# Kernel optimization log

Hardware: AMD Instinct MI355X
Metric: run time of the kernel (lower is better)

Reference implementation:

```python
import jax, jax.numpy as jnp
import numpy as np

B = 32768
D = 1024          # input_dim
SEL = 512         # select_dim (per-expert selected features)
E = 6             # num_experts
K = 3             # top_k
SH = 32           # shared_dim
INNER = 64        # cross-attn inner dim (4 heads * 16)
HID = 128         # expert hidden


def setup_inputs() -> dict:
    key = jax.random.key(0)
    ks = jax.random.split(key, 16)
    s = lambda i, shape, scale=0.02: (jax.random.normal(ks[i], shape, jnp.float32) * scale)
    return {
        "x": jax.random.normal(ks[0], (B, D), jnp.float32),
        # CrossAttention(query_dim=512, context_dim=512, heads=4, dim_head=16)
        "Wq": s(1, (512, INNER)),
        "Wk": s(2, (512, INNER)),
        "Wv": s(3, (512, INNER)),
        "Wo": s(4, (INNER, 512)),
        "bo": jnp.zeros((512,), jnp.float32),
        # shared_proj: Linear(512, 32)
        "Wsp": s(5, (512, SH)),
        "bsp": jnp.zeros((SH,), jnp.float32),
        # gate: Linear(1024, 6)
        "Wg": s(6, (D, E)),
        "bg": jnp.zeros((E,), jnp.float32),
        # per-expert feature-mask logits
        "mask_logits": jax.random.normal(ks[7], (E, D), jnp.float32),
        # expert MLPs: Linear(544,128) -> ReLU -> Linear(128,1), stacked over experts
        "W1": s(8, (E, SEL + SH, HID)),
        "b1": jnp.zeros((E, HID), jnp.float32),
        "W2": s(9, (E, HID, 1)),
        "b2": jnp.zeros((E, 1), jnp.float32),
    }


def _moe_forward(x, Wq, Wk, Wv, Wo, bo, Wsp, bsp, Wg, bg, mask_logits, W1, b1, W2, b2):
    x_sem = x[:, :512]
    x_vis = x[:, 512:]

    # CrossAttention with a single query token attending to a single context
    # token: softmax over one key is identically 1, so attn output == v.
    v = x_vis @ Wv                      # [B, INNER]
    shared_token = v @ Wo + bo          # to_out Linear, [B, 512]
    shared_info = shared_token @ Wsp + bsp  # [B, SH]

    # Gating: top-k experts per sample, softmax over selected logits
    gate_logits = x @ Wg + bg                       # [B, E]
    topk_scores, topk_idx = jax.lax.top_k(gate_logits, K)  # [B, K]
    topk_w = jax.nn.softmax(topk_scores, axis=1)    # [B, K]

    # Per-expert learned feature selection (top-512 of sigmoid(mask_logits));
    # sigmoid is monotonic but kept for faithfulness.
    mask_prob = jax.nn.sigmoid(mask_logits)         # [E, D]
    _, sel_idx = jax.lax.top_k(mask_prob, SEL)      # [E, SEL]

    # Dense expert evaluation (every expert on every sample), then gather the
    # routed outputs -- same math as the original scatter loop.
    x_sel = jnp.take(x, sel_idx, axis=1)            # [B, E, SEL]
    h = jnp.einsum('bes,esh->beh', x_sel, W1[:, :SEL, :])
    h = h + jnp.einsum('bd,edh->beh', shared_info, W1[:, SEL:, :])
    h = jax.nn.relu(h + b1[None])                   # [B, E, HID]
    expert_out = jnp.einsum('beh,eh->be', h, W2[:, :, 0]) + b2[None, :, 0]  # [B, E]

    routed = jnp.take_along_axis(expert_out, topk_idx, axis=1)  # [B, K]
    return jnp.sum(topk_w * routed, axis=1, keepdims=True)      # [B, 1]


def reference(x, Wq, Wk, Wv, Wo, bo, Wsp, bsp, Wg, bg, mask_logits, W1, b1, W2, b2):
    return _moe_forward(x, Wq, Wk, Wv, Wo, bo, Wsp, bsp, Wg, bg, mask_logits, W1, b1, W2, b2)
```

## Files before the change

### kernel.cpp

```cpp
#include <hip/hip_runtime.h>

#define B 32768
#define D 1024
#define SEL 512
#define E 6
#define K 3
#define SH 32
#define HID 128
#define NKT 16

typedef __attribute__((ext_vector_type(8))) short bf16x8;
typedef __attribute__((ext_vector_type(4))) float f32x4;

__device__ __forceinline__ unsigned short f2bf(float f) {
  unsigned u = __float_as_uint(f);
  return (unsigned short)((u + 0x7fffu + ((u >> 16) & 1u)) >> 16);
}
__device__ __forceinline__ float bf2f(unsigned short h) {
  return __uint_as_float((unsigned)h << 16);
}

__device__ __forceinline__ void gload_lds16(const void* g, void* l) {
  __builtin_amdgcn_global_load_lds(
      (const __attribute__((address_space(1))) void*)g,
      (__attribute__((address_space(3))) void*)l, 16, 0, 0);
}

__global__ void k_sel(const float* __restrict__ ml, int* __restrict__ inv,
                      int* __restrict__ cnt) {
  __shared__ float row[D];
  const int e = blockIdx.x, t = threadIdx.x;
  if (t == 0) cnt[e] = 0;
  row[t] = ml[e * D + t];
  __syncthreads();
  const float v = row[t];
  int rank = 0;
  for (int i = 0; i < D; ++i) {
    float u = row[i];
    rank += (u > v) || (u == v && i < t);
  }
  inv[e * D + t] = (rank < SEL) ? rank : -1;
}

__global__ __launch_bounds__(256) void k_wowsp(
    const float* __restrict__ Wo, const float* __restrict__ Wsp,
    const float* __restrict__ bo, const float* __restrict__ bsp,
    const float* __restrict__ Wg,
    float* __restrict__ WoWsp, float* __restrict__ bfull,
    unsigned short* __restrict__ WgS) {
  __shared__ float red[256];
  const int t = threadIdx.x;
  const int j = t & 31, chunk = t >> 5;
  const int blk = blockIdx.x;
  if (blk < 64) {
    const int i = blk;
    float p = 0.f;
    for (int c = chunk * 64; c < chunk * 64 + 64; ++c)
      p += Wo[i * 512 + c] * Wsp[c * SH + j];
    red[t] = p;
    __syncthreads();
    if (t < 32) {
      float s = 0.f;
      #pragma unroll
      for (int k = 0; k < 8; ++k) s += red[k * 32 + j];
      WoWsp[i * SH + j] = s;
    }
  } else if (blk == 64) {
    float p = 0.f;
    for (int c = chunk * 64; c < chunk * 64 + 64; ++c)
      p += bo[c] * Wsp[c * SH + j];
    red[t] = p;
    __syncthreads();
    if (t < 32) {
      float s = bsp[j];
      #pragma unroll
      for (int k = 0; k < 8; ++k) s += red[k * 32 + j];
      bfull[j] = s;
    }
  } else {
    const int idx = (blk - 65) * 256 + t;
    const int col = idx >> 10, k = idx & 1023;
    float wv = (col < E) ? Wg[(size_t)k * E + col] : 0.f;
    unsigned short hi = f2bf(wv);
    unsigned short lo = f2bf(wv - bf2f(hi));
    WgS[col * D + k] = hi;
    WgS[16 * D + col * D + k] = lo;
  }
}

__global__ __launch_bounds__(256) void k_wfull2(
    const float* __restrict__ Wv, const float* __restrict__ WoWsp,
    float* __restrict__ Wfull) {
  __shared__ float wsh[64 * SH];
  const int t = threadIdx.x;
  for (int idx = t; idx < 64 * SH; idx += 256) wsh[idx] = WoWsp[idx];
  __syncthreads();
  const int c = blockIdx.x * 8 + (t >> 5), j = t & 31;
  float p = 0.f;
  #pragma unroll 8
  for (int i = 0; i < 64; ++i) p += Wv[c * 64 + i] * wsh[i * SH + j];
  Wfull[c * SH + j] = p;
}

__global__ __launch_bounds__(256) void k_w1c(
    const float* __restrict__ W1, const float* __restrict__ b1,
    const int* __restrict__ inv, const float* __restrict__ Wfull,
    const float* __restrict__ bfull,
    unsigned short* __restrict__ W1eT, float* __restrict__ b1c) {
  __shared__ float w1b[SH];
  __shared__ float bf[SH];
  const int e = blockIdx.x >> 7, h = blockIdx.x & 127;
  const int t = threadIdx.x;
  const float* We = W1 + (size_t)e * (SEL + SH) * HID;
  if (t < SH) { w1b[t] = We[(size_t)(SEL + t) * HID + h]; bf[t] = bfull[t]; }
  __syncthreads();
  const int* iv = inv + e * D;
  unsigned short* dst = W1eT + ((size_t)e * HID + h) * D;
  #pragma unroll
  for (int it = 0; it < 4; ++it) {
    int d = t + it * 256;
    int s = iv[d];
    float v = (s >= 0) ? We[(size_t)s * HID + h] : 0.f;
    if (d >= 512) {
      const float* wf = Wfull + (size_t)(d - 512) * SH;
      float p = 0.f;
      #pragma unroll
      for (int j = 0; j < SH; ++j) p += wf[j] * w1b[j];
      v += p;
    }
    dst[d] = f2bf(v);
  }
  if (t == 0) {
    float p = b1[e * HID + h];
    for (int j = 0; j < SH; ++j) p += bf[j] * w1b[j];
    b1c[e * HID + h] = p;
  }
}

template<bool WRITE_XBF>
__global__ __launch_bounds__(256) void k_xgate(
    const float* __restrict__ x, const unsigned short* __restrict__ WgS,
    const float* __restrict__ Wg, const float* __restrict__ bg,
    unsigned short* __restrict__ xbf,
    int* __restrict__ cnt, int* __restrict__ clist, float* __restrict__ wlist) {
  __shared__ __align__(16) char ldsAh[64 * 128];
  __shared__ __align__(16) char ldsAl[64 * 128];
  __shared__ __align__(16) char ldsW[4096];
  __shared__ float gl_s[64][8];
  const int t = threadIdx.x;
  const int bm = blockIdx.x;
  const int w = t >> 6, lane = t & 63;
  const int g = lane >> 4, j = lane & 15;
  const int swz = ((lane & 7) * 16) ^ ((lane >> 3) << 4);

  const char* srcW = (const char*)WgS +
                     (size_t)(w * 8 + (lane >> 3)) * (D * 2) + swz;

  f32x4 acc = {0.f, 0.f, 0.f, 0.f};

  for (int kt = 0; kt < NKT; ++kt) {
    if (kt) __syncthreads();
    gload_lds16(srcW + kt * 128, ldsW + w * 1024);
    #pragma unroll
    for (int it = 0; it < 4; ++it) {
      int r = (t >> 4) + it * 16;
      const float4 v =
          *(const float4*)(x + (size_t)(bm * 64 + r) * D + kt * 64 + (t & 15) * 4);
      ushort4 hh, ll;
      hh.x = f2bf(v.x); hh.y = f2bf(v.y); hh.z = f2bf(v.z); hh.w = f2bf(v.w);
      ll.x = f2bf(v.x - bf2f(hh.x)); ll.y = f2bf(v.y - bf2f(hh.y));
      ll.z = f2bf(v.z - bf2f(hh.z)); ll.w = f2bf(v.w - bf2f(hh.w));
      if (WRITE_XBF)
        *(ushort4*)(xbf + (size_t)(bm * 64 + r) * D + kt * 64 + (t & 15) * 4) = hh;
      const int ao = r * 128 + (((t & 15) * 8) ^ ((r & 7) << 4));
      *(ushort4*)(ldsAh + ao) = hh;
      *(ushort4*)(ldsAl + ao) = ll;
    }
    __syncthreads();
    #pragma unroll
    for (int kk = 0; kk < 2; ++kk) {
      const int kb = kk * 64 + g * 16;
      const int wo = kb ^ ((j & 7) << 4);
      bf16x8 bh = *(const bf16x8*)(ldsW + j * 128 + wo);
      bf16x8 bl = *(const bf16x8*)(ldsW + 2048 + j * 128 + wo);
      const int row = w * 16 + j;
      const int aoff = row * 128 + (kb ^ ((row & 7) << 4));
      bf16x8 ah = *(const bf16x8*)(ldsAh + aoff);
      bf16x8 al = *(const bf16x8*)(ldsAl + aoff);
      acc = __builtin_amdgcn_mfma_f32_16x16x32_bf16(ah, bh, acc, 0, 0, 0);
      acc = __builtin_amdgcn_mfma_f32_16x16x32_bf16(ah, bl, acc, 0, 0, 0);
      acc = __builtin_amdgcn_mfma_f32_16x16x32_bf16(al, bh, acc, 0, 0, 0);
      acc = __builtin_amdgcn_mfma_f32_16x16x32_bf16(al, bl, acc, 0, 0, 0);
    }
  }
  if (j < E) {
    #pragma unroll
    for (int ri = 0; ri < 4; ++ri)
      gl_s[w * 16 + g * 4 + ri][j] = acc[ri];
  }
  __syncthreads();
  if (t < 64) {
    const int tok = bm * 64 + t;
    float gv[E];
    #pragma unroll
    for (int e2 = 0; e2 < E; ++e2) gv[e2] = gl_s[t][e2] + bg[e2];

    float s4[4];
    {
      bool used[E] = {};
      #pragma unroll
      for (int k = 0; k < 4; ++k) {
        float best = -1e30f; int bi = 0;
        for (int e2 = 0; e2 < E; ++e2)
          if (!used[e2] && gv[e2] > best) { best = gv[e2]; bi = e2; }
        used[bi] = true; s4[k] = best;
      }
    }
    unsigned long long flags = __ballot(s4[2] - s4[3] < 4e-3f);
    while (flags) {
      const int fl = __ffsll((long long)flags) - 1;
      flags &= flags - 1;
      const int tokf = bm * 64 + fl;
      float ex[E] = {};
      for (int i = 0; i < 16; ++i) {
        const int d = t + 64 * i;
        float xv = x[(size_t)tokf * D + d];
        const float* wr = Wg + (size_t)d * E;
        #pragma unroll
        for (int e2 = 0; e2 < E; ++e2) ex[e2] += xv * wr[e2];
      }
      #pragma unroll
      for (int e2 = 0; e2 < E; ++e2) {
        float s = ex[e2];
        s += __shfl_xor(s, 1); s += __shfl_xor(s, 2); s += __shfl_xor(s, 4);
        s += __shfl_xor(s, 8); s += __shfl_xor(s, 16); s += __shfl_xor(s, 32);
        ex[e2] = s;
      }
      if (t == fl) {
        #pragma unroll
        for (int e2 = 0; e2 < E; ++e2) gv[e2] = ex[e2] + bg[e2];
      }
    }
    int idx[K]; float sc[K];
    bool used[E] = {};
    #pragma unroll
    for (int k = 0; k < K; ++k) {
      float best = -1e30f; int bi = 0;
      for (int e2 = 0; e2 < E; ++e2)
        if (!used[e2] && gv[e2] > best) { best = gv[e2]; bi = e2; }
      used[bi] = true; sc[k] = best; idx[k] = bi;
    }
    float s1 = __expf(sc[1] - sc[0]), s2 = __expf(sc[2] - sc[0]);
    float inv_s = 1.f / (1.f + s1 + s2);
    float tw[K] = {inv_s, s1 * inv_s, s2 * inv_s};
    const unsigned long long below = (1ULL << t) - 1ULL;
    #pragma unroll
    for (int e2 = 0; e2 < E; ++e2) {
      int myk = -1;
      #pragma unroll
      for (int k = 0; k < K; ++k) if (idx[k] == e2) myk = k;
      unsigned long long m = __ballot(myk >= 0);
      if (m) {
        int tot = __popcll(m);
        int leader = __ffsll((long long)m) - 1;
        int base = 0;
        if (t == leader) base = atomicAdd(&cnt[e2], tot);
        base = __shfl(base, leader);
        if (myk >= 0) {
          int pos = base + __popcll(m & below);
          clist[e2 * B + pos] = (tok << 2) | myk;
          wlist[e2 * B + pos] = tw[myk];
        }
      }
    }
  }
}

template<int AMODE>
__global__ __launch_bounds__(256) void k_gemm(
    const float* __restrict__ x, const unsigned short* __restrict__ xbf,
    const unsigned short* __restrict__ W1eT,
    const int* __restrict__ cnt, const int* __restrict__ clist,
    const float* __restrict__ wlist,
    const float* __restrict__ b1c, const float* __restrict__ W2,
    const float* __restrict__ b2, float* __restrict__ eo4) {
  __shared__ __align__(16) char ldsA[128 * 128];
  __shared__ __align__(16) char ldsB[128 * 128];
  __shared__ int tokl[128];
  __shared__ float red[128];

  const int t = threadIdx.x;
  const int e = blockIdx.x >> 8;
  const int bm = blockIdx.x & 255;
  const int n = cnt[e];
  if (bm * 128 >= n) return;
  const int cb = e * B;

  if (t < 128) {
    int gr = bm * 128 + t;
    tokl[t] = clist[cb + (gr < n ? gr : 0)] >> 2;
  }
  __syncthreads();

  const int w = t >> 6, lane = t & 63;
  const int g = lane >> 4, j = lane & 15;
  const int swz = ((lane & 7) * 16) ^ ((lane >> 3) << 4);

  const char* srcB[4];
  #pragma unroll
  for (int q = 0; q < 4; ++q)
    srcB[q] = (const char*)W1eT +
              (size_t)(e * HID + w * 32 + q * 8 + (lane >> 3)) * (D * 2) + swz;
  const char* srcA[4];
  if (AMODE == 0) {
    #pragma unroll
    for (int q = 0; q < 4; ++q)
      srcA[q] = (const char*)xbf +
                (size_t)tokl[w * 32 + q * 8 + (lane >> 3)] * 2048 + swz;
  }

  f32x4 acc[2][8] = {};

  for (int kt = 0; kt < NKT; ++kt) {
    if (kt) __syncthreads();
    if (AMODE == 0) {
      #pragma unroll
      for (int q = 0; q < 4; ++q)
        gload_lds16(srcA[q] + kt * 128, ldsA + w * 4096 + q * 1024);
    }
    #pragma unroll
    for (int q = 0; q < 4; ++q)
      gload_lds16(srcB[q] + kt * 128, ldsB + w * 4096 + q * 1024);
    if (AMODE == 1) {
      #pragma unroll
      for (int it = 0; it < 8; ++it) {
        int r = (t >> 4) + it * 16;
        const float4 v =
            *(const float4*)(x + (size_t)tokl[r] * D + kt * 64 + (t & 15) * 4);
        ushort4 h4;
        h4.x = f2bf(v.x); h4.y = f2bf(v.y); h4.z = f2bf(v.z); h4.w = f2bf(v.w);
        *(ushort4*)(ldsA + r * 128 + (((t & 15) * 8) ^ ((r & 7) << 4))) = h4;
      }
    }
    __syncthreads();
    #pragma unroll
    for (int kk = 0; kk < 2; ++kk) {
      const int kb = kk * 64 + g * 16;
      bf16x8 aF[2];
      #pragma unroll
      for (int fm = 0; fm < 2; ++fm) {
        int row = w * 32 + fm * 16 + j;
        aF[fm] = *(const bf16x8*)(ldsA + row * 128 + (kb ^ ((row & 7) << 4)));
      }
      #pragma unroll
      for (int fn = 0; fn < 8; ++fn) {
        int col = fn * 16 + j;
        bf16x8 bF = *(const bf16x8*)(ldsB + col * 128 + (kb ^ ((col & 7) << 4)));
        acc[0][fn] = __builtin_amdgcn_mfma_f32_16x16x32_bf16(aF[0], bF, acc[0][fn], 0, 0, 0);
        acc[1][fn] = __builtin_amdgcn_mfma_f32_16x16x32_bf16(aF[1], bF, acc[1][fn], 0, 0, 0);
      }
    }
  }

  float vb1[8], vw2[8];
  #pragma unroll
  for (int fn = 0; fn < 8; ++fn) {
    int col = fn * 16 + j;
    vb1[fn] = b1c[e * HID + col];
    vw2[fn] = W2[e * HID + col];
  }
  #pragma unroll
  for (int fm = 0; fm < 2; ++fm) {
    #pragma unroll
    for (int r = 0; r < 4; ++r) {
      float s = 0.f;
      #pragma unroll
      for (int fn = 0; fn < 8; ++fn)
        s += fmaxf(acc[fm][fn][r] + vb1[fn], 0.f) * vw2[fn];
      s += __shfl_xor(s, 1); s += __shfl_xor(s, 2);
      s += __shfl_xor(s, 4); s += __shfl_xor(s, 8);
      if (j == 0) red[w * 32 + fm * 16 + g * 4 + r] = s;
    }
  }
  __syncthreads();
  if (t < 128) {
    int gr = bm * 128 + t;
    if (gr < n) {
      int en = clist[cb + gr];
      eo4[(size_t)(en >> 2) * 4 + (en & 3)] = wlist[cb + gr] * (red[t] + b2[e]);
    }
  }
}

__global__ void k_comb2(const float* __restrict__ eo4, float* __restrict__ out) {
  const int tok = blockIdx.x * 256 + threadIdx.x;
  float4 v = *(const float4*)(eo4 + (size_t)tok * 4);
  out[tok] = v.x + v.y + v.z;
}

extern "C" void kernel_launch(void* const* d_in, const int* in_sizes, int n_in,
                              void* d_out, int out_size, void* d_ws, size_t ws_size,
                              hipStream_t stream) {
  const float* x   = (const float*)d_in[0];
  const float* Wv  = (const float*)d_in[3];
  const float* Wo  = (const float*)d_in[4];
  const float* bo  = (const float*)d_in[5];
  const float* Wsp = (const float*)d_in[6];
  const float* bsp = (const float*)d_in[7];
  const float* Wg  = (const float*)d_in[8];
  const float* bg  = (const float*)d_in[9];
  const float* ml  = (const float*)d_in[10];
  const float* W1  = (const float*)d_in[11];
  const float* b1  = (const float*)d_in[12];
  const float* W2  = (const float*)d_in[13];
  const float* b2  = (const float*)d_in[14];
  float* out = (float*)d_out;

  char* ws = (char*)d_ws;
  int*   inv   = (int*)ws;
  float* WoWsp = (float*)(ws + 32768);
  float* Wfull = (float*)(ws + 49152);
  float* bfull = (float*)(ws + 114688);
  float* b1c   = (float*)(ws + 118784);
  int*   cnt   = (int*)(ws + 126976);
  unsigned short* WgS = (unsigned short*)(ws + 131072);
  int*   clist = (int*)(ws + 262144);
  float* wlist = (float*)(ws + 1048576);
  float* eo4   = (float*)(ws + 1835008);
  unsigned short* W1eT = (unsigned short*)(ws + 2359296);
  unsigned short* xbf  = (unsigned short*)(ws + 3932160);
  const bool use_xbf = ws_size >= (size_t)3932160 + (size_t)B * D * 2;

  k_sel<<<E, D, 0, stream>>>(ml, inv, cnt);
  k_wowsp<<<129, 256, 0, stream>>>(Wo, Wsp, bo, bsp, Wg, WoWsp, bfull, WgS);
  k_wfull2<<<64, 256, 0, stream>>>(Wv, WoWsp, Wfull);
  k_w1c<<<E * HID, 256, 0, stream>>>(W1, b1, inv, Wfull, bfull, W1eT, b1c);
  if (use_xbf)
    k_xgate<true><<<B / 64, 256, 0, stream>>>(x, WgS, Wg, bg, xbf, cnt, clist, wlist);
  else
    k_xgate<false><<<B / 64, 256, 0, stream>>>(x, WgS, Wg, bg, xbf, cnt, clist, wlist);
  if (use_xbf)
    k_gemm<0><<<E * 256, 256, 0, stream>>>(x, xbf, W1eT, cnt, clist, wlist, b1c, W2, b2, eo4);
  else
    k_gemm<1><<<E * 256, 256, 0, stream>>>(x, xbf, W1eT, cnt, clist, wlist, b1c, W2, b2, eo4);
  k_comb2<<<B / 256, 256, 0, stream>>>(eo4, out);
}
```

Measured before the change: 175.7 us.

## Software-pipeline x and gate-weight loads in the gating kernel

The gating kernel now issues the next k-tile's x float4 loads into registers and its gate-weight tile into a second LDS buffer before running the MFMA work on the current tile. This replaces the old load-then-compute sequence inside each iteration. The goal is to hide global memory latency on the large x read behind the bf16 split and MFMA math. In exchange it uses more registers and an extra 4 KB of LDS, which may reduce occupancy.

```diff
diff --git a/kernel.cpp b/kernel.cpp
--- a/kernel.cpp
+++ b/kernel.cpp
@@ -145,44 +145,66 @@
     int* __restrict__ cnt, int* __restrict__ clist, float* __restrict__ wlist) {
   __shared__ __align__(16) char ldsAh[64 * 128];
   __shared__ __align__(16) char ldsAl[64 * 128];
-  __shared__ __align__(16) char ldsW[4096];
+  __shared__ __align__(16) char ldsW[2][4096];
   __shared__ float gl_s[64][8];
   const int t = threadIdx.x;
   const int bm = blockIdx.x;
   const int w = t >> 6, lane = t & 63;
   const int g = lane >> 4, j = lane & 15;
+  const int tok0 = bm * 64;
   const int swz = ((lane & 7) * 16) ^ ((lane >> 3) << 4);
+  const int r0 = t >> 4, c16 = t & 15;
 
   const char* srcW = (const char*)WgS +
                      (size_t)(w * 8 + (lane >> 3)) * (D * 2) + swz;
 
   f32x4 acc = {0.f, 0.f, 0.f, 0.f};
 
+  gload_lds16(srcW, ldsW[0] + w * 1024);
+  float4 vb0, vb1, vb2, vb3;
+  {
+    const float* xp = x + (size_t)(tok0 + r0) * D + c16 * 4;
+    vb0 = *(const float4*)(xp);
+    vb1 = *(const float4*)(xp + 16 * D);
+    vb2 = *(const float4*)(xp + 32 * D);
+    vb3 = *(const float4*)(xp + 48 * D);
+  }
+
   for (int kt = 0; kt < NKT; ++kt) {
     if (kt) __syncthreads();
-    gload_lds16(srcW + kt * 128, ldsW + w * 1024);
-    #pragma unroll
-    for (int it = 0; it < 4; ++it) {
-      int r = (t >> 4) + it * 16;
-      const float4 v =
-          *(const float4*)(x + (size_t)(bm * 64 + r) * D + kt * 64 + (t & 15) * 4);
-      ushort4 hh, ll;
-      hh.x = f2bf(v.x); hh.y = f2bf(v.y); hh.z = f2bf(v.z); hh.w = f2bf(v.w);
-      ll.x = f2bf(v.x - bf2f(hh.x)); ll.y = f2bf(v.y - bf2f(hh.y));
-      ll.z = f2bf(v.z - bf2f(hh.z)); ll.w = f2bf(v.w - bf2f(hh.w));
-      if (WRITE_XBF)
-        *(ushort4*)(xbf + (size_t)(bm * 64 + r) * D + kt * 64 + (t & 15) * 4) = hh;
-      const int ao = r * 128 + (((t & 15) * 8) ^ ((r & 7) << 4));
-      *(ushort4*)(ldsAh + ao) = hh;
-      *(ushort4*)(ldsAl + ao) = ll;
+    {
+      float4 vv[4] = {vb0, vb1, vb2, vb3};
+      #pragma unroll
+      for (int it = 0; it < 4; ++it) {
+        const int r = r0 + it * 16;
+        float4 v = vv[it];
+        ushort4 hh, ll;
+        hh.x = f2bf(v.x); hh.y = f2bf(v.y); hh.z = f2bf(v.z); hh.w = f2bf(v.w);
+        ll.x = f2bf(v.x - bf2f(hh.x)); ll.y = f2bf(v.y - bf2f(hh.y));
+        ll.z = f2bf(v.z - bf2f(hh.z)); ll.w = f2bf(v.w - bf2f(hh.w));
+        if (WRITE_XBF)
+          *(ushort4*)(xbf + (size_t)(tok0 + r) * D + kt * 64 + c16 * 4) = hh;
+        const int ao = r * 128 + ((c16 * 8) ^ ((r & 7) << 4));
+        *(ushort4*)(ldsAh + ao) = hh;
+        *(ushort4*)(ldsAl + ao) = ll;
+      }
     }
     __syncthreads();
+    if (kt + 1 < NKT) {
+      gload_lds16(srcW + (kt + 1) * 128, ldsW[(kt + 1) & 1] + w * 1024);
+      const float* xp = x + (size_t)(tok0 + r0) * D + (kt + 1) * 64 + c16 * 4;
+      vb0 = *(const float4*)(xp);
+      vb1 = *(const float4*)(xp + 16 * D);
+      vb2 = *(const float4*)(xp + 32 * D);
+      vb3 = *(const float4*)(xp + 48 * D);
+    }
+    const char* Wcur = ldsW[kt & 1];
     #pragma unroll
     for (int kk = 0; kk < 2; ++kk) {
       const int kb = kk * 64 + g * 16;
       const int wo = kb ^ ((j & 7) << 4);
-      bf16x8 bh = *(const bf16x8*)(ldsW + j * 128 + wo);
-      bf16x8 bl = *(const bf16x8*)(ldsW + 2048 + j * 128 + wo);
+      bf16x8 bh = *(const bf16x8*)(Wcur + j * 128 + wo);
+      bf16x8 bl = *(const bf16x8*)(Wcur + 2048 + j * 128 + wo);
       const int row = w * 16 + j;
       const int aoff = row * 128 + (kb ^ ((row & 7) << 4));
       bf16x8 ah = *(const bf16x8*)(ldsAh + aoff);
```

New measurement: 175.8 us, median of 2. About the same (+0.0%).
